# Kernel optimization log

Measured on AMD Instinct MI355X. Metric: run time of the kernel, lower is better.

Reference implementation:

```python
import jax, jax.numpy as jnp
import numpy as np

D_HEAD = 64

def setup_inputs() -> dict:
    key = jax.random.key(0)
    k1, k2, k3, k4, k5 = jax.random.split(key, 5)
    b, s, d_model, n_heads, d_head = 2, 4096, 512, 8, D_HEAD
    x = jax.random.normal(k1, (b, s, d_model), dtype=jnp.float32)
    scale = 1.0 / np.sqrt(d_model)
    W_K = jax.random.normal(k2, (n_heads, d_head, d_model), dtype=jnp.float32) * scale
    W_Q = jax.random.normal(k3, (n_heads, d_head, d_model), dtype=jnp.float32) * scale
    W_V = jax.random.normal(k4, (n_heads, d_head, d_model), dtype=jnp.float32) * scale
    W_O = jax.random.normal(k5, (d_model, d_head * n_heads), dtype=jnp.float32) * scale
    return {"x": x, "W_K": W_K, "W_Q": W_Q, "W_V": W_V, "W_O": W_O}

def reference(x, W_K, W_Q, W_V, W_O):
    # x: [b, p, d]; W_{K,Q,V}: [i, h, d]; W_O: [d, i*h]
    s = x.shape[-2]
    k = jnp.einsum('ihd,bpd->biph', W_K, x)
    q = jnp.einsum('ihd,bpd->biph', W_Q, x)
    v = jnp.einsum('ihd,bpd->biph', W_V, x)
    scores = jnp.einsum('biph,biqh->biqp', k, q)  # [b, i, q, p]
    mask = jnp.tril(jnp.ones((s, s), dtype=scores.dtype))
    scores = jnp.tril(scores) - 1e10 * (1.0 - mask)
    attn = jax.nn.softmax(scores / np.sqrt(D_HEAD), axis=-1)
    z = jnp.einsum('biph,biqp->biqh', v, attn)  # [b, i, q, h]
    b, i, qlen, h = z.shape
    z_flat = jnp.transpose(z, (0, 2, 1, 3)).reshape(b, qlen, i * h)  # 'b i q h -> b q (i h)'
    out = jnp.einsum('df,bqf->bqd', W_O, z_flat)
    return out
```

## Files before the change

### kernel.cpp

```cpp
#include <hip/hip_runtime.h>
#include <hip/hip_bf16.h>


typedef __attribute__((ext_vector_type(4)))  float  f32x4;
typedef __attribute__((ext_vector_type(16))) float  f32x16;
typedef __attribute__((ext_vector_type(8)))  __bf16 bf16x8;
typedef __attribute__((ext_vector_type(8)))  unsigned short u16x8;
typedef __attribute__((ext_vector_type(4)))  unsigned int u32x4;

#define MFMA16(a, b, c) __builtin_amdgcn_mfma_f32_16x16x32_bf16((a), (b), (c), 0, 0, 0)
#define MFMA32(a, b, c) __builtin_amdgcn_mfma_f32_32x32x16_bf16((a), (b), (c), 0, 0, 0)
#define SWZ(g, r) ((g) ^ ((r) & 7))
#define SLOTS_BH 72

static __device__ __forceinline__ bf16x8 ld8(const __hip_bfloat16* p) {
    return *reinterpret_cast<const bf16x8*>(p);
}
static __device__ __forceinline__ __hip_bfloat16 tobf(float f) {
    return __float2bfloat16(f);
}
static __device__ __forceinline__ float exp2_raw(float x) {
    float r;
    asm("v_exp_f32 %0, %1" : "=v"(r) : "v"(x));
    return r;
}
static __device__ __forceinline__ unsigned cvt_pk(float lo, float hi) {
    unsigned r;
    asm("v_cvt_pk_bf16_f32 %0, %1, %2" : "=v"(r) : "v"(lo), "v"(hi));
    return r;
}
static __device__ __forceinline__ void pl32swap(unsigned& a, unsigned& b) {
    asm("v_permlane32_swap_b32 %0, %1" : "+v"(a), "+v"(b));
}
static __device__ __forceinline__ void gl_lds16(const __hip_bfloat16* g, __hip_bfloat16* l) {
    typedef __attribute__((address_space(1))) const unsigned int GU;
    typedef __attribute__((address_space(3))) unsigned int LU;
    __builtin_amdgcn_global_load_lds((GU*)(const void*)g, (LU*)(void*)l, 16, 0, 0);
}
static __device__ __forceinline__ int nchunks(int qi) { return (qi + 2) >> 1; }
static __device__ __forceinline__ int slot_off(int qi) {
    const int a = qi >> 1;
    return (qi & 1) ? (a + 1) * (a + 1) : a * a + a;
}

__global__ __launch_bounds__(256) void cast_all(
    const float* __restrict__ x,  const float* __restrict__ wk,
    const float* __restrict__ wq, const float* __restrict__ wv,
    const float* __restrict__ wo,
    __hip_bfloat16* __restrict__ xb,  __hip_bfloat16* __restrict__ wkb,
    __hip_bfloat16* __restrict__ wqb, __hip_bfloat16* __restrict__ wvb,
    __hip_bfloat16* __restrict__ wob)
{
    const int bid = blockIdx.x;
    const float* src;
    __hip_bfloat16* dst;
    int base;
    if (bid < 2048) { src = x; dst = xb; base = bid; }
    else {
        const int r = (bid - 2048) >> 7;
        base = (bid - 2048) & 127;
        src = (r == 0) ? wk : (r == 1) ? wq : (r == 2) ? wv : wo;
        dst = (r == 0) ? wkb : (r == 1) ? wqb : (r == 2) ? wvb : wob;
    }
    const size_t i = (size_t)base * 256 + threadIdx.x;
    const float4 a = *reinterpret_cast<const float4*>(src + i * 8);
    const float4 b = *reinterpret_cast<const float4*>(src + i * 8 + 4);
    u16x8 o;
    o[0] = __bfloat16_as_ushort(tobf(a.x));
    o[1] = __bfloat16_as_ushort(tobf(a.y));
    o[2] = __bfloat16_as_ushort(tobf(a.z));
    o[3] = __bfloat16_as_ushort(tobf(a.w));
    o[4] = __bfloat16_as_ushort(tobf(b.x));
    o[5] = __bfloat16_as_ushort(tobf(b.y));
    o[6] = __bfloat16_as_ushort(tobf(b.z));
    o[7] = __bfloat16_as_ushort(tobf(b.w));
    *reinterpret_cast<u16x8*>(dst + i * 8) = o;
}

__global__ __launch_bounds__(512) void qkv_gemm(
    const __hip_bfloat16* __restrict__ x,
    const __hip_bfloat16* __restrict__ Wk,
    const __hip_bfloat16* __restrict__ Wq,
    const __hip_bfloat16* __restrict__ Wv,
    __hip_bfloat16* __restrict__ Qo,
    __hip_bfloat16* __restrict__ Ko,
    __hip_bfloat16* __restrict__ Vt)
{
    __shared__ __hip_bfloat16 Xlds[2][128][64];
    __shared__ __hip_bfloat16 Wlds[2][128][64];

    const int mt = blockIdx.x;
    const int ni = blockIdx.y;
    const int z  = ni >> 2;
    const int m0 = mt * 128;

    const __hip_bfloat16* Wz =
        (z == 0 ? Wk : (z == 1 ? Wq : Wv)) + (size_t)(ni & 3) * 128 * 512;

    const int tid  = threadIdx.x;
    const int w    = tid >> 6;
    const int lane = tid & 63;
    const int q31  = lane & 31;
    const int hi   = lane >> 5;
    const int wm   = w >> 1;
    const int wn   = w & 1;

    const int r0l = w * 8 + (lane >> 3);
    const int cg  = (lane & 7) ^ (r0l & 7);
    const __hip_bfloat16* Xsrc = x  + (size_t)(m0 + r0l) * 512 + cg * 8;
    const __hip_bfloat16* Wsrc = Wz + (size_t)r0l * 512 + cg * 8;

    auto stage = [&](int buf, int k0) {
        gl_lds16(Xsrc + k0,                    &Xlds[buf][w * 8][0]);
        gl_lds16(Xsrc + k0 + (size_t)64 * 512, &Xlds[buf][w * 8 + 64][0]);
        gl_lds16(Wsrc + k0,                    &Wlds[buf][w * 8][0]);
        gl_lds16(Wsrc + k0 + (size_t)64 * 512, &Wlds[buf][w * 8 + 64][0]);
    };

    const int ra  = wm * 32 + q31;
    const int rb0 = wn * 64 + q31;
    const int rb1 = wn * 64 + 32 + q31;
    int gA[4], gB0[4], gB1[4];
#pragma unroll
    for (int ks = 0; ks < 4; ++ks) {
        gA[ks]  = SWZ(2 * ks + hi, ra)  * 8;
        gB0[ks] = SWZ(2 * ks + hi, rb0) * 8;
        gB1[ks] = SWZ(2 * ks + hi, rb1) * 8;
    }

    f32x16 ac0 = {}, ac1 = {};
    stage(0, 0);

    for (int it = 0; it < 8; ++it) {
        const int buf = it & 1;
        asm volatile("s_waitcnt vmcnt(0)" ::: "memory");
        __syncthreads();
        if (it < 7) stage(buf ^ 1, (it + 1) * 64);

        const __hip_bfloat16* xa  = &Xlds[buf][ra][0];
        const __hip_bfloat16* wb0 = &Wlds[buf][rb0][0];
        const __hip_bfloat16* wb1 = &Wlds[buf][rb1][0];

        __builtin_amdgcn_s_setprio(1);
#pragma unroll
        for (int ks = 0; ks < 4; ++ks) {
            bf16x8 a  = *(const bf16x8*)(xa  + gA[ks]);
            bf16x8 b0 = *(const bf16x8*)(wb0 + gB0[ks]);
            bf16x8 b1 = *(const bf16x8*)(wb1 + gB1[ks]);
            ac0 = MFMA32(a, b0, ac0);
            ac1 = MFMA32(a, b1, ac1);
        }
        __builtin_amdgcn_s_setprio(0);
    }

    const int b     = m0 >> 12;
    const int sbase = (m0 & 4095) + wm * 32;
    const int hc0   = (ni & 3) * 128 + wn * 64;

    if (z == 2) {
        auto vstore = [&](const f32x16& ac, int cf) {
            const int hcol = hc0 + cf * 32 + q31;
            const int h = hcol >> 6, dh = hcol & 63;
            __hip_bfloat16* vbase =
                Vt + ((size_t)(b * 8 + h) * 64 + dh) * 4096;
#pragma unroll
            for (int q2 = 0; q2 < 4; ++q2) {
                ushort4 pk;
                pk.x = __bfloat16_as_ushort(tobf(ac[q2 * 4 + 0]));
                pk.y = __bfloat16_as_ushort(tobf(ac[q2 * 4 + 1]));
                pk.z = __bfloat16_as_ushort(tobf(ac[q2 * 4 + 2]));
                pk.w = __bfloat16_as_ushort(tobf(ac[q2 * 4 + 3]));
                *reinterpret_cast<ushort4*>(vbase + sbase + 8 * q2 + 4 * hi) = pk;
            }
        };
        vstore(ac0, 0);
        vstore(ac1, 1);
    } else {
        const float scale = (z == 1) ? 0.18033688f : 1.0f;
        __hip_bfloat16* O = (z == 0) ? Ko : Qo;
        auto kstore = [&](const f32x16& ac, int cf) {
            const int hcol = hc0 + cf * 32 + q31;
            const int h = hcol >> 6, dh = hcol & 63;
            __hip_bfloat16* obase =
                O + (size_t)(b * 8 + h) * 4096 * 64 + dh;
#pragma unroll
            for (int reg = 0; reg < 16; ++reg) {
                const int srow = sbase + (reg & 3) + 8 * (reg >> 2) + 4 * hi;
                obase[(size_t)srow * 64] = tobf(ac[reg] * scale);
            }
        };
        kstore(ac0, 0);
        kstore(ac1, 1);
    }
}

__global__ __launch_bounds__(512) void attn_part(
    const __hip_bfloat16* __restrict__ Q,
    const __hip_bfloat16* __restrict__ K,
    const __hip_bfloat16* __restrict__ Vt,
    __hip_bfloat16* __restrict__ Zp,
    float* __restrict__ ML,
    __hip_bfloat16* __restrict__ Z)
{
    __shared__ __hip_bfloat16 Klds[2][64][64];
    __shared__ __hip_bfloat16 Vlds[2][64][64];
    __shared__ float als[8][32];

    const int id = blockIdx.x;
    const int bh = ((id & 7) << 1) | ((id >> 3) & 1);
    int rem = id >> 4;
    int qi = 15;
    for (;;) { const int ncq = nchunks(qi); if (rem < ncq) break; rem -= ncq; --qi; }
    const int c  = rem;
    const int nc = nchunks(qi);

    const int w    = threadIdx.x >> 6;
    const int lane = threadIdx.x & 63;
    const int q31  = lane & 31;
    const int hi   = lane >> 5;

    const __hip_bfloat16* Qb = Q  + (size_t)bh * 4096 * 64;
    const __hip_bfloat16* Kb = K  + (size_t)bh * 4096 * 64;
    const __hip_bfloat16* Vb = Vt + (size_t)bh * 64 * 4096;

    const int wbase = qi * 256 + w * 32;
    const int qrow  = wbase + q31;
    const int wqmax = wbase + 31;

    bf16x8 qf[4];
#pragma unroll
    for (int ks = 0; ks < 4; ++ks)
        qf[ks] = ld8(Qb + (size_t)qrow * 64 + ks * 16 + hi * 8);

    f32x16 za0 = {}, za1 = {};
    float l_ln = 0.0f;

    const int t0   = c * 8;
    const int tend = min(t0 + 8, 4 * qi + 4);
    const int nt   = tend - t0;

    int gsx[4];
#pragma unroll
    for (int ks = 0; ks < 4; ++ks) gsx[ks] = SWZ(2 * ks + hi, q31) * 8;

    const int r0l = w * 8 + (lane >> 3);
    const int cg  = (lane & 7) ^ (r0l & 7);
    const __hip_bfloat16* Ksrc = Kb + (size_t)r0l * 64 + cg * 8;
    const __hip_bfloat16* Vsrc = Vb + (size_t)r0l * 4096 + cg * 8;

    auto stage = [&](int buf, int t) {
        const int p0 = t * 64;
        gl_lds16(Ksrc + (size_t)p0 * 64, &Klds[buf][w * 8][0]);
        gl_lds16(Vsrc + p0,              &Vlds[buf][w * 8][0]);
    };

    stage(0, t0);

    for (int it = 0; it < nt; ++it) {
        const int t   = t0 + it;
        const int buf = it & 1;

        asm volatile("s_waitcnt vmcnt(0)" ::: "memory");
        __syncthreads();
        if (it + 1 < nt) stage(buf ^ 1, t + 1);

        const int p0 = t * 64;
        if (p0 > wqmax) continue;

        const __hip_bfloat16* kb0 = &Klds[buf][q31][0];
        const __hip_bfloat16* kb1 = &Klds[buf][32 + q31][0];

        f32x16 sa0 = {}, sa1 = {};
        __builtin_amdgcn_s_setprio(1);
#pragma unroll
        for (int ks = 0; ks < 4; ++ks) {
            bf16x8 k0 = *(const bf16x8*)(kb0 + gsx[ks]);
            bf16x8 k1 = *(const bf16x8*)(kb1 + gsx[ks]);
            sa0 = MFMA32(k0, qf[ks], sa0);
            sa1 = MFMA32(k1, qf[ks], sa1);
        }
        __builtin_amdgcn_s_setprio(0);

        if (p0 + 63 > wbase) {
#pragma unroll
            for (int reg = 0; reg < 16; ++reg) {
                const int pl = (reg & 3) + 8 * (reg >> 2) + 4 * hi;
                const int p  = p0 + pl;
                sa0[reg] = (p      <= qrow) ? sa0[reg] : -1.0e30f;
                sa1[reg] = (p + 32 <= qrow) ? sa1[reg] : -1.0e30f;
            }
        }

#pragma unroll
        for (int reg = 0; reg < 16; ++reg) {
            sa0[reg] = exp2_raw(sa0[reg]);
            sa1[reg] = exp2_raw(sa1[reg]);
        }

        float ts[8];
#pragma unroll
        for (int i = 0; i < 8; ++i)
            ts[i] = (sa0[i] + sa0[i + 8]) + (sa1[i] + sa1[i + 8]);
#pragma unroll
        for (int s = 4; s; s >>= 1)
#pragma unroll
            for (int i = 0; i < s; ++i) ts[i] += ts[i + s];
        l_ln += ts[0];

        bf16x8 pfrag[4];
#pragma unroll
        for (int kb = 0; kb < 4; ++kb) {
            const int e = (kb & 1) * 8;
            unsigned px, py, pu, pv;
            if (kb < 2) {
                px = cvt_pk(sa0[e + 0], sa0[e + 1]);
                py = cvt_pk(sa0[e + 2], sa0[e + 3]);
                pu = cvt_pk(sa0[e + 4], sa0[e + 5]);
                pv = cvt_pk(sa0[e + 6], sa0[e + 7]);
            } else {
                px = cvt_pk(sa1[e + 0], sa1[e + 1]);
                py = cvt_pk(sa1[e + 2], sa1[e + 3]);
                pu = cvt_pk(sa1[e + 4], sa1[e + 5]);
                pv = cvt_pk(sa1[e + 6], sa1[e + 7]);
            }
            pl32swap(px, pu);
            pl32swap(py, pv);
            u32x4 fw;
            fw[0] = px; fw[1] = py; fw[2] = pu; fw[3] = pv;
            pfrag[kb] = __builtin_bit_cast(bf16x8, fw);
        }

        const __hip_bfloat16* vb0 = &Vlds[buf][q31][0];
        const __hip_bfloat16* vb1 = &Vlds[buf][32 + q31][0];

        __builtin_amdgcn_s_setprio(1);
#pragma unroll
        for (int kb = 0; kb < 4; ++kb) {
            bf16x8 v0 = *(const bf16x8*)(vb0 + gsx[kb]);
            bf16x8 v1 = *(const bf16x8*)(vb1 + gsx[kb]);
            za0 = MFMA32(pfrag[kb], v0, za0);
            za1 = MFMA32(pfrag[kb], v1, za1);
        }
        __builtin_amdgcn_s_setprio(0);
    }

    float lt = l_ln + __shfl_xor(l_ln, 32);

    if (nc == 1) {
        if (hi == 0) als[w][q31] = 1.0f / lt;
        const int b = bh >> 3, h = bh & 7;
#pragma unroll
        for (int reg = 0; reg < 16; ++reg) {
            const int q = (reg & 3) + 8 * (reg >> 2) + 4 * hi;
            const float inv = als[w][q];
            __hip_bfloat16* zo =
                Z + ((size_t)b * 4096 + qi * 256 + w * 32 + q) * 512 + h * 64 + q31;
            zo[0]  = tobf(za0[reg] * inv);
            zo[32] = tobf(za1[reg] * inv);
        }
    } else {
        const int slot = bh * SLOTS_BH + slot_off(qi) + c;
        if (hi == 0) {
            ML[(size_t)slot * 512 +       w * 32 + q31] = 0.0f;
            ML[(size_t)slot * 512 + 256 + w * 32 + q31] = lt;
        }
#pragma unroll
        for (int reg = 0; reg < 16; ++reg) {
            const int q = (reg & 3) + 8 * (reg >> 2) + 4 * hi;
            const size_t base =
                (size_t)slot * 16384 + (size_t)(w * 32 + q) * 64 + q31;
            Zp[base]      = tobf(za0[reg]);
            Zp[base + 32] = tobf(za1[reg]);
        }
    }
}

__global__ __launch_bounds__(512) void attn_combine(
    const __hip_bfloat16* __restrict__ Zp,
    const float* __restrict__ ML,
    __hip_bfloat16* __restrict__ Z)
{
    const int qi = blockIdx.x + 2;
    const int bh = blockIdx.y;
    const int nc = nchunks(qi);
    const int q    = threadIdx.x >> 1;
    const int half = threadIdx.x & 1;

    const int slot0 = bh * SLOTS_BH + slot_off(qi);

    float M = -3.0e38f;
    for (int i = 0; i < nc; ++i)
        M = fmaxf(M, ML[(size_t)(slot0 + i) * 512 + q]);

    float L = 0.0f;
    float acc[32];
#pragma unroll
    for (int j = 0; j < 32; ++j) acc[j] = 0.0f;

    for (int i = 0; i < nc; ++i) {
        const float wgt = exp2_raw(ML[(size_t)(slot0 + i) * 512 + q] - M);
        L += wgt * ML[(size_t)(slot0 + i) * 512 + 256 + q];
        const __hip_bfloat16* zp =
            Zp + (size_t)(slot0 + i) * 16384 + (size_t)q * 64 + half * 32;
#pragma unroll
        for (int v = 0; v < 4; ++v) {
            bf16x8 z = ld8(zp + v * 8);
#pragma unroll
            for (int j = 0; j < 8; ++j) acc[v * 8 + j] += wgt * (float)z[j];
        }
    }

    const float inv = 1.0f / L;
    const int b = bh >> 3, h = bh & 7;
    __hip_bfloat16* zo =
        Z + ((size_t)b * 4096 + qi * 256 + q) * 512 + h * 64 + half * 32;
#pragma unroll
    for (int v = 0; v < 4; ++v) {
        u16x8 o;
#pragma unroll
        for (int j = 0; j < 8; ++j)
            o[j] = __bfloat16_as_ushort(tobf(acc[v * 8 + j] * inv));
        *reinterpret_cast<u16x8*>(zo + v * 8) = o;
    }
}

__global__ __launch_bounds__(512) void out_gemm(
    const __hip_bfloat16* __restrict__ Zf,
    const __hip_bfloat16* __restrict__ Wo,
    float* __restrict__ out)
{
    __shared__ __hip_bfloat16 Alds[2][128][64];
    __shared__ __hip_bfloat16 Blds[2][128][64];

    const int mt = blockIdx.x;
    const int ni = blockIdx.y;
    const int m0 = mt * 128;
    const int n0 = ni * 128;

    const int tid  = threadIdx.x;
    const int w    = tid >> 6;
    const int lane = tid & 63;
    const int q31  = lane & 31;
    const int hi   = lane >> 5;
    const int wm   = w >> 1;
    const int wn   = w & 1;

    const int r0l = w * 8 + (lane >> 3);
    const int cg  = (lane & 7) ^ (r0l & 7);
    const __hip_bfloat16* Asrc = Zf + (size_t)(m0 + r0l) * 512 + cg * 8;
    const __hip_bfloat16* Bsrc = Wo + (size_t)(n0 + r0l) * 512 + cg * 8;

    auto stage = [&](int buf, int k0) {
        gl_lds16(Asrc + k0,                    &Alds[buf][w * 8][0]);
        gl_lds16(Asrc + k0 + (size_t)64 * 512, &Alds[buf][w * 8 + 64][0]);
        gl_lds16(Bsrc + k0,                    &Blds[buf][w * 8][0]);
        gl_lds16(Bsrc + k0 + (size_t)64 * 512, &Blds[buf][w * 8 + 64][0]);
    };

    const int ra  = wm * 32 + q31;
    const int rb0 = wn * 64 + q31;
    const int rb1 = wn * 64 + 32 + q31;
    int gA[4], gB0[4], gB1[4];
#pragma unroll
    for (int ks = 0; ks < 4; ++ks) {
        gA[ks]  = SWZ(2 * ks + hi, ra)  * 8;
        gB0[ks] = SWZ(2 * ks + hi, rb0) * 8;
        gB1[ks] = SWZ(2 * ks + hi, rb1) * 8;
    }

    f32x16 ac0 = {}, ac1 = {};
    stage(0, 0);

    for (int it = 0; it < 8; ++it) {
        const int buf = it & 1;
        asm volatile("s_waitcnt vmcnt(0)" ::: "memory");
        __syncthreads();
        if (it < 7) stage(buf ^ 1, (it + 1) * 64);

        const __hip_bfloat16* xa  = &Alds[buf][ra][0];
        const __hip_bfloat16* wb0 = &Blds[buf][rb0][0];
        const __hip_bfloat16* wb1 = &Blds[buf][rb1][0];

        __builtin_amdgcn_s_setprio(1);
#pragma unroll
        for (int ks = 0; ks < 4; ++ks) {
            bf16x8 a  = *(const bf16x8*)(xa  + gA[ks]);
            bf16x8 b0 = *(const bf16x8*)(wb0 + gB0[ks]);
            bf16x8 b1 = *(const bf16x8*)(wb1 + gB1[ks]);
            ac0 = MFMA32(a, b0, ac0);
            ac1 = MFMA32(a, b1, ac1);
        }
        __builtin_amdgcn_s_setprio(0);
    }

    const int row0 = m0 + wm * 32;
    const int col0 = n0 + wn * 64;
#pragma unroll
    for (int reg = 0; reg < 16; ++reg) {
        const int r = row0 + (reg & 3) + 8 * (reg >> 2) + 4 * hi;
        out[(size_t)r * 512 + col0 + q31]      = ac0[reg];
        out[(size_t)r * 512 + col0 + 32 + q31] = ac1[reg];
    }
}

extern "C" void kernel_launch(void* const* d_in, const int* in_sizes, int n_in,
                              void* d_out, int out_size, void* d_ws, size_t ws_size,
                              hipStream_t stream)
{
    const float* x_f  = (const float*)d_in[0];
    const float* Wk_f = (const float*)d_in[1];
    const float* Wq_f = (const float*)d_in[2];
    const float* Wv_f = (const float*)d_in[3];
    const float* Wo_f = (const float*)d_in[4];
    float* out = (float*)d_out;

    char* ws = (char*)d_ws;
    const size_t szQKV = (size_t)16 * 4096 * 64 * sizeof(__hip_bfloat16);
    const size_t szX   = (size_t)8192 * 512 * sizeof(__hip_bfloat16);
    const size_t szW   = (size_t)8 * 64 * 512 * sizeof(__hip_bfloat16);
    const size_t szZp  = (size_t)16 * SLOTS_BH * 256 * 64 * sizeof(__hip_bfloat16);
    const size_t szML  = (size_t)16 * SLOTS_BH * 512 * sizeof(float);

    size_t off = 0;
    __hip_bfloat16* Qb  = (__hip_bfloat16*)(ws + off); off += szQKV;
    __hip_bfloat16* Kb  = (__hip_bfloat16*)(ws + off); off += szQKV;
    __hip_bfloat16* Vt  = (__hip_bfloat16*)(ws + off); off += szQKV;
    __hip_bfloat16* Zb  = (__hip_bfloat16*)(ws + off); off += szX;
    __hip_bfloat16* Wob = (__hip_bfloat16*)(ws + off); off += szW;
    const size_t trans = off;
    __hip_bfloat16* xb  = (__hip_bfloat16*)(ws + trans);
    __hip_bfloat16* Wkb = (__hip_bfloat16*)(ws + trans + szX);
    __hip_bfloat16* Wqb = (__hip_bfloat16*)(ws + trans + szX + szW);
    __hip_bfloat16* Wvb = (__hip_bfloat16*)(ws + trans + szX + 2 * szW);
    __hip_bfloat16* Zp  = (__hip_bfloat16*)(ws + trans);
    float*          ML  = (float*)(ws + trans + szZp);

    cast_all<<<2048 + 4 * 128, 256, 0, stream>>>(
        x_f, Wk_f, Wq_f, Wv_f, Wo_f, xb, Wkb, Wqb, Wvb, Wob);

    qkv_gemm<<<dim3(64, 12),    512, 0, stream>>>(xb, Wkb, Wqb, Wvb, Qb, Kb, Vt);
    attn_part<<<dim3(1152),     512, 0, stream>>>(Qb, Kb, Vt, Zp, ML, Zb);
    attn_combine<<<dim3(14, 16), 512, 0, stream>>>(Zp, ML, Zb);
    out_gemm<<<dim3(64, 4),     512, 0, stream>>>(Zb, Wob, out);
}
```

Measured before the change: 102.3 us.

## Double attention block to 1024 threads so 16 waves share K/V tiles

The attention-partial kernel now processes 512 query rows per block with 16 waves instead of 256 rows with 8 waves, and launches half as many blocks. Waves 0-7 stage K tiles and waves 8-15 stage V tiles, so each K/V tile brought into LDS is reused by twice as many query rows. Every chunk now runs a fixed 8 key tiles, and the slot indexing is remapped so the combine kernel still finds its partials. The costs are tighter register limits at 1024 threads per block, and the lower-half waves idle on diagonal tiles their rows never attend to.

Measured after the change: 106.2 us. 3.8% more time.

```diff
diff --git a/kernel.cpp b/kernel.cpp
--- a/kernel.cpp
+++ b/kernel.cpp
@@ -37,10 +37,10 @@
     typedef __attribute__((address_space(3))) unsigned int LU;
     __builtin_amdgcn_global_load_lds((GU*)(const void*)g, (LU*)(void*)l, 16, 0, 0);
 }
-static __device__ __forceinline__ int nchunks(int qi) { return (qi + 2) >> 1; }
-static __device__ __forceinline__ int slot_off(int qi) {
-    const int a = qi >> 1;
-    return (qi & 1) ? (a + 1) * (a + 1) : a * a + a;
+static __device__ __forceinline__ int nchunks(int q2) { return (q2 + 2) >> 1; }
+static __device__ __forceinline__ int slot_off(int q2) {
+    const int a = q2 >> 1;
+    return (q2 & 1) ? (a + 1) * (a + 1) : a * a + a;
 }
 
 __global__ __launch_bounds__(256) void cast_all(
@@ -194,7 +194,7 @@
     }
 }
 
-__global__ __launch_bounds__(512) void attn_part(
+__global__ __launch_bounds__(1024) void attn_part(
     const __hip_bfloat16* __restrict__ Q,
     const __hip_bfloat16* __restrict__ K,
     const __hip_bfloat16* __restrict__ Vt,
@@ -204,15 +204,14 @@
 {
     __shared__ __hip_bfloat16 Klds[2][64][64];
     __shared__ __hip_bfloat16 Vlds[2][64][64];
-    __shared__ float als[8][32];
+    __shared__ float als[16][32];
 
     const int id = blockIdx.x;
     const int bh = ((id & 7) << 1) | ((id >> 3) & 1);
     int rem = id >> 4;
-    int qi = 15;
-    for (;;) { const int ncq = nchunks(qi); if (rem < ncq) break; rem -= ncq; --qi; }
-    const int c  = rem;
-    const int nc = nchunks(qi);
+    int qi = 7;
+    for (;;) { const int ncq = qi + 1; if (rem < ncq) break; rem -= ncq; --qi; }
+    const int c = rem;
 
     const int w    = threadIdx.x >> 6;
     const int lane = threadIdx.x & 63;
@@ -223,9 +222,11 @@
     const __hip_bfloat16* Kb = K  + (size_t)bh * 4096 * 64;
     const __hip_bfloat16* Vb = Vt + (size_t)bh * 64 * 4096;
 
-    const int wbase = qi * 256 + w * 32;
+    const int wbase = qi * 512 + w * 32;
     const int qrow  = wbase + q31;
     const int wqmax = wbase + 31;
+    const int Q2    = 2 * qi + (w >> 3);
+    const int nc    = qi + 1;
 
     bf16x8 qf[4];
 #pragma unroll
@@ -235,34 +236,34 @@
     f32x16 za0 = {}, za1 = {};
     float l_ln = 0.0f;
 
-    const int t0   = c * 8;
-    const int tend = min(t0 + 8, 4 * qi + 4);
-    const int nt   = tend - t0;
+    const int t0 = c * 8;
 
     int gsx[4];
 #pragma unroll
     for (int ks = 0; ks < 4; ++ks) gsx[ks] = SWZ(2 * ks + hi, q31) * 8;
 
-    const int r0l = w * 8 + (lane >> 3);
+    const int r0l = (w & 7) * 8 + (lane >> 3);
     const int cg  = (lane & 7) ^ (r0l & 7);
-    const __hip_bfloat16* Ksrc = Kb + (size_t)r0l * 64 + cg * 8;
-    const __hip_bfloat16* Vsrc = Vb + (size_t)r0l * 4096 + cg * 8;
+    const bool kside = (w < 8);
+    const __hip_bfloat16* src =
+        kside ? Kb + (size_t)r0l * 64 + cg * 8
+              : Vb + (size_t)r0l * 4096 + cg * 8;
 
     auto stage = [&](int buf, int t) {
         const int p0 = t * 64;
-        gl_lds16(Ksrc + (size_t)p0 * 64, &Klds[buf][w * 8][0]);
-        gl_lds16(Vsrc + p0,              &Vlds[buf][w * 8][0]);
+        if (kside) gl_lds16(src + (size_t)p0 * 64, &Klds[buf][(w & 7) * 8][0]);
+        else       gl_lds16(src + p0,              &Vlds[buf][(w & 7) * 8][0]);
     };
 
     stage(0, t0);
 
-    for (int it = 0; it < nt; ++it) {
+    for (int it = 0; it < 8; ++it) {
         const int t   = t0 + it;
         const int buf = it & 1;
 
         asm volatile("s_waitcnt vmcnt(0)" ::: "memory");
         __syncthreads();
-        if (it + 1 < nt) stage(buf ^ 1, t + 1);
+        if (it + 1 < 8) stage(buf ^ 1, t + 1);
 
         const int p0 = t * 64;
         if (p0 > wqmax) continue;
@@ -345,6 +346,7 @@
     }
 
     float lt = l_ln + __shfl_xor(l_ln, 32);
+    const int hrow = (w & 7) * 32;
 
     if (nc == 1) {
         if (hi == 0) als[w][q31] = 1.0f / lt;
@@ -354,21 +356,21 @@
             const int q = (reg & 3) + 8 * (reg >> 2) + 4 * hi;
             const float inv = als[w][q];
             __hip_bfloat16* zo =
-                Z + ((size_t)b * 4096 + qi * 256 + w * 32 + q) * 512 + h * 64 + q31;
+                Z + ((size_t)b * 4096 + wbase + q) * 512 + h * 64 + q31;
             zo[0]  = tobf(za0[reg] * inv);
             zo[32] = tobf(za1[reg] * inv);
         }
     } else {
-        const int slot = bh * SLOTS_BH + slot_off(qi) + c;
+        const int slot = bh * SLOTS_BH + slot_off(Q2) + c;
         if (hi == 0) {
-            ML[(size_t)slot * 512 +       w * 32 + q31] = 0.0f;
-            ML[(size_t)slot * 512 + 256 + w * 32 + q31] = lt;
+            ML[(size_t)slot * 512 +       hrow + q31] = 0.0f;
+            ML[(size_t)slot * 512 + 256 + hrow + q31] = lt;
         }
 #pragma unroll
         for (int reg = 0; reg < 16; ++reg) {
             const int q = (reg & 3) + 8 * (reg >> 2) + 4 * hi;
             const size_t base =
-                (size_t)slot * 16384 + (size_t)(w * 32 + q) * 64 + q31;
+                (size_t)slot * 16384 + (size_t)(hrow + q) * 64 + q31;
             Zp[base]      = tobf(za0[reg]);
             Zp[base + 32] = tobf(za1[reg]);
         }
@@ -539,7 +541,7 @@
         x_f, Wk_f, Wq_f, Wv_f, Wo_f, xb, Wkb, Wqb, Wvb, Wob);
 
     qkv_gemm<<<dim3(64, 12),    512, 0, stream>>>(xb, Wkb, Wqb, Wvb, Qb, Kb, Vt);
-    attn_part<<<dim3(1152),     512, 0, stream>>>(Qb, Kb, Vt, Zp, ML, Zb);
+    attn_part<<<dim3(576),     1024, 0, stream>>>(Qb, Kb, Vt, Zp, ML, Zb);
     attn_combine<<<dim3(14, 16), 512, 0, stream>>>(Zp, ML, Zb);
     out_gemm<<<dim3(64, 4),     512, 0, stream>>>(Zb, Wob, out);
 }
```
